# Kernel tuning notes

Measured on AMD Instinct MI355X. Metric: run time of the kernel, lower is better.

Reference implementation:

```python
import jax, jax.numpy as jnp
import numpy as np

EMBED_DIM = 1024
VOCAB = 32000
B, S = 4, 4096


def setup_inputs() -> dict:
    key = jax.random.key(0)
    ks = jax.random.split(key, 6)
    scale = 1.0 / np.sqrt(EMBED_DIM)
    x = jax.random.randint(ks[0], (B, S), 0, VOCAB, dtype=jnp.int64)
    embed = jax.random.normal(ks[1], (VOCAB, EMBED_DIM), dtype=jnp.float32)
    qkv_w = jax.random.normal(ks[2], (EMBED_DIM, 3 * EMBED_DIM), dtype=jnp.float32) * scale
    qkv_b = jnp.zeros((3 * EMBED_DIM,), dtype=jnp.float32)
    out_w = jax.random.normal(ks[3], (EMBED_DIM, VOCAB), dtype=jnp.float32) * scale
    out_b = jnp.zeros((VOCAB,), dtype=jnp.float32)
    return {"x": x, "embed": embed, "qkv_w": qkv_w, "qkv_b": qkv_b,
            "out_w": out_w, "out_b": out_b}


def reference(x, embed, qkv_w, qkv_b, out_w, out_b):
    h = embed[x]                                   # [B,S,D] token embedding lookup
    qkv = h @ qkv_w + qkv_b                        # [B,S,3D]
    qkv = qkv.reshape(B, S, 3, EMBED_DIM)
    q, k, v = qkv[:, :, 0], qkv[:, :, 1], qkv[:, :, 2]
    logits = jnp.einsum('bqd,bkd->bqk', q, k) / jnp.sqrt(jnp.float32(EMBED_DIM))
    attn = jax.nn.softmax(logits, axis=-1)         # [B,S,S] full score matrix (as in source)
    out = jnp.einsum('bqk,bkd->bqd', attn, v)
    h = out + h                                    # residual
    # source applies output projection then slices last token; equivalent to
    # projecting the last-token hidden only.
    return h[:, -1, :] @ out_w + out_b             # [B, vocab]
```

## Files before the change

kernel.cpp:

```cpp
#include <hip/hip_runtime.h>
#include <hip/hip_bf16.h>

typedef __bf16 bf16;
typedef __bf16 bf16x4 __attribute__((ext_vector_type(4)));
typedef __bf16 bf16x8 __attribute__((ext_vector_type(8)));
typedef float floatx4 __attribute__((ext_vector_type(4)));

#define EMBED 1024
#define VOCAB 32000
#define BB    4
#define SS    4096
#define NTOK  (BB * SS)
#define NKV   2048
#define NSEG  16

__device__ __forceinline__ void async_copy16(void* lds, const void* g) {
    __builtin_amdgcn_global_load_lds(
        (const __attribute__((address_space(1))) unsigned int*)g,
        (__attribute__((address_space(3))) unsigned int*)lds, 16, 0, 0);
}

__global__ void gather_embed(const int* __restrict__ x,
                             const float* __restrict__ embed,
                             bf16* __restrict__ h,
                             float* __restrict__ h_last,
                             float* __restrict__ h_final) {
    int t = blockIdx.x;
    int tid = threadIdx.x;
    int row = x[t];
    const float4* src = (const float4*)(embed + (size_t)row * EMBED);
    float4 v = src[tid];
    bf16x4 o; o.x = (bf16)v.x; o.y = (bf16)v.y; o.z = (bf16)v.z; o.w = (bf16)v.w;
    *(bf16x4*)(h + (size_t)t * EMBED + tid * 4) = o;
    if ((t & (SS - 1)) == SS - 1) {
        int b = t >> 12;
        *(float4*)(h_last  + b * EMBED + tid * 4) = v;
        *(float4*)(h_final + b * EMBED + tid * 4) = v;
    }
}

__global__ void wkvt_transpose(const float* __restrict__ qkv_w,
                               bf16* __restrict__ WkvT) {
    __shared__ float T[32][33];
    int n0 = blockIdx.x * 32, d0 = blockIdx.y * 32;
    int tid = threadIdx.x;
    int c = tid & 31, r = tid >> 5;
#pragma unroll
    for (int i = 0; i < 4; ++i) {
        int d = r + i * 8;
        T[c][d] = qkv_w[(size_t)(d0 + d) * (3 * EMBED) + EMBED + n0 + c];
    }
    __syncthreads();
#pragma unroll
    for (int i = 0; i < 4; ++i) {
        int n = r + i * 8;
        WkvT[(size_t)(n0 + n) * EMBED + d0 + c] = (bf16)T[n][c];
    }
}

__global__ void q_gemm(const float* __restrict__ h_last,
                       const float* __restrict__ qkv_w,
                       float* __restrict__ qpart) {
    __shared__ float hs[BB * 64];
    int tid = threadIdx.x;
    int seg = blockIdx.x, d0 = seg * 64;
    hs[tid] = h_last[(tid >> 6) * EMBED + d0 + (tid & 63)];
    __syncthreads();
    int j0 = tid * 4;
    floatx4 acc[BB];
#pragma unroll
    for (int b = 0; b < BB; ++b) acc[b] = (floatx4)0.0f;
#pragma unroll 4
    for (int dd = 0; dd < 64; ++dd) {
        float4 w = *(const float4*)(qkv_w + (size_t)(d0 + dd) * (3 * EMBED) + j0);
#pragma unroll
        for (int b = 0; b < BB; ++b) {
            float hv = hs[b * 64 + dd];
            acc[b][0] += hv * w.x; acc[b][1] += hv * w.y;
            acc[b][2] += hv * w.z; acc[b][3] += hv * w.w;
        }
    }
#pragma unroll
    for (int b = 0; b < BB; ++b)
        *(floatx4*)(qpart + ((size_t)seg * BB + b) * EMBED + j0) = acc[b];
}

__global__ void q_reduce(const float* __restrict__ qpart,
                         const float* __restrict__ qkv_b,
                         float* __restrict__ q) {
    int k = blockIdx.x * 256 + threadIdx.x;
    int b = k >> 10, d = k & (EMBED - 1);
    float s = qkv_b[d];
#pragma unroll
    for (int sg = 0; sg < NSEG; ++sg) s += qpart[((size_t)sg * BB + b) * EMBED + d];
    q[k] = s;
}

__global__ __launch_bounds__(512, 2) void gemm_kv(
    const bf16* __restrict__ A,
    const bf16* __restrict__ BT,
    const float* __restrict__ bias,
    bf16* __restrict__ C) {
    __shared__ __align__(16) bf16 SA[2][2][256 * 32];
    __shared__ __align__(16) bf16 SB[2][2][256 * 32];

    const int tid  = threadIdx.x;
    const int wave = tid >> 6, lane = tid & 63;
    const int wm = wave >> 2, wn = wave & 3;
    const int l16 = lane & 15, quad = lane >> 4;
    const int swz_l = (l16 & 3) ^ ((l16 >> 2) & 3);
    const int a_base = (wm * 128 + l16) * 32 + (quad ^ swz_l) * 8;
    const int b_base = (wn * 64  + l16) * 32 + (quad ^ swz_l) * 8;

    const bf16* Abase = A  + (size_t)blockIdx.x * 256 * EMBED;
    const bf16* Bbase = BT + (size_t)blockIdx.y * 256 * EMBED;

    floatx4 acc[8][4];
#pragma unroll
    for (int m = 0; m < 8; ++m)
#pragma unroll
        for (int n = 0; n < 4; ++n) acc[m][n] = (floatx4)0.0f;

    bf16x8 af[4], bfr[4];

#define STAGE_A(HALF, KT) do { \
    int c_ = wave * 128 + lane; \
    int r_ = c_ >> 2, sw_ = (r_ & 3) ^ ((r_ >> 2) & 3); \
    async_copy16(&SA[HALF][(KT) & 1][c_ * 8], \
        Abase + (size_t)r_ * EMBED + (KT) * 64 + (HALF) * 32 + ((c_ & 3) ^ sw_) * 8); \
    c_ += 64; r_ = c_ >> 2; sw_ = (r_ & 3) ^ ((r_ >> 2) & 3); \
    async_copy16(&SA[HALF][(KT) & 1][c_ * 8], \
        Abase + (size_t)r_ * EMBED + (KT) * 64 + (HALF) * 32 + ((c_ & 3) ^ sw_) * 8); \
} while (0)

#define STAGE_B(HALF, KT) do { \
    int c_ = wave * 128 + lane; \
    int r_ = c_ >> 2, sw_ = (r_ & 3) ^ ((r_ >> 2) & 3); \
    async_copy16(&SB[HALF][(KT) & 1][c_ * 8], \
        Bbase + (size_t)r_ * EMBED + (KT) * 64 + (HALF) * 32 + ((c_ & 3) ^ sw_) * 8); \
    c_ += 64; r_ = c_ >> 2; sw_ = (r_ & 3) ^ ((r_ >> 2) & 3); \
    async_copy16(&SB[HALF][(KT) & 1][c_ * 8], \
        Bbase + (size_t)r_ * EMBED + (KT) * 64 + (HALF) * 32 + ((c_ & 3) ^ sw_) * 8); \
} while (0)

#define RD_A(KS, PAR, MH) do { \
    const bf16* pa_ = &SA[KS][PAR][a_base + (MH) * 2048]; \
    _Pragma("unroll") \
    for (int mf_ = 0; mf_ < 4; ++mf_) af[mf_] = *(const bf16x8*)(pa_ + mf_ * 512); \
} while (0)

#define RD_B(KS, PAR) do { \
    const bf16* pb_ = &SB[KS][PAR][b_base]; \
    _Pragma("unroll") \
    for (int nf_ = 0; nf_ < 4; ++nf_) bfr[nf_] = *(const bf16x8*)(pb_ + nf_ * 512); \
} while (0)

#define MFMA16(MH) do { \
    __builtin_amdgcn_s_setprio(1); \
    _Pragma("unroll") \
    for (int mf_ = 0; mf_ < 4; ++mf_) \
    _Pragma("unroll") \
    for (int nf_ = 0; nf_ < 4; ++nf_) \
        acc[(MH) * 4 + mf_][nf_] = __builtin_amdgcn_mfma_f32_16x16x32_bf16( \
            af[mf_], bfr[nf_], acc[(MH) * 4 + mf_][nf_], 0, 0, 0); \
    __builtin_amdgcn_s_setprio(0); \
} while (0)

#define BARLG() do { __builtin_amdgcn_s_barrier(); \
    asm volatile("s_waitcnt lgkmcnt(0)" ::: "memory"); } while (0)
#define BAR()   __builtin_amdgcn_s_barrier()
#define WAIT8() do { __builtin_amdgcn_sched_barrier(0); \
    asm volatile("s_waitcnt vmcnt(8)" ::: "memory"); } while (0)
#define WAIT4() do { __builtin_amdgcn_sched_barrier(0); \
    asm volatile("s_waitcnt vmcnt(4)" ::: "memory"); } while (0)
#define WAIT0() do { __builtin_amdgcn_sched_barrier(0); \
    asm volatile("s_waitcnt vmcnt(0)" ::: "memory"); } while (0)
#define NOSTG() do { } while (0)

#define GROUP(PAR, S1, S2, S3, S4, W2, W4) do { \
    RD_A(0, PAR, 0); RD_B(0, PAR); S1; BARLG(); MFMA16(0); BAR(); \
    RD_A(0, PAR, 1);               S2; BARLG(); MFMA16(1); W2; BAR(); \
    RD_A(1, PAR, 0); RD_B(1, PAR); S3; BARLG(); MFMA16(0); BAR(); \
    RD_A(1, PAR, 1);               S4; BARLG(); MFMA16(1); W4; BAR(); \
} while (0)

    STAGE_A(0, 0); STAGE_B(0, 0);
    STAGE_A(1, 0); STAGE_B(1, 0);
    STAGE_A(0, 1); STAGE_B(0, 1);
    __builtin_amdgcn_sched_barrier(0);
    asm volatile("s_waitcnt vmcnt(8)" ::: "memory");
    BAR();

#pragma unroll 1
    for (int kk = 0; kk < 7; ++kk) {
        const int k0 = kk * 2, k1 = k0 + 1;
        GROUP(0, STAGE_A(1, k0 + 1), STAGE_B(1, k0 + 1),
                 STAGE_A(0, k0 + 2), STAGE_B(0, k0 + 2), WAIT8(), WAIT8());
        GROUP(1, STAGE_A(1, k1 + 1), STAGE_B(1, k1 + 1),
                 STAGE_A(0, k1 + 2), STAGE_B(0, k1 + 2), WAIT8(), WAIT8());
    }
    GROUP(0, STAGE_A(1, 15), STAGE_B(1, 15), NOSTG(), NOSTG(), WAIT8(), WAIT4());
    GROUP(1, NOSTG(), NOSTG(), NOSTG(), NOSTG(), WAIT0(), NOSTG());

    const int crow0 = blockIdx.x * 256 + wm * 128;
    const int ccol0 = blockIdx.y * 256 + wn * 64;
    float bsv[4];
#pragma unroll
    for (int nf = 0; nf < 4; ++nf) bsv[nf] = bias[ccol0 + nf * 16 + l16];
#pragma unroll
    for (int fm = 0; fm < 8; ++fm)
#pragma unroll
        for (int nf = 0; nf < 4; ++nf) {
            int col = ccol0 + nf * 16 + l16;
#pragma unroll
            for (int r = 0; r < 4; ++r) {
                int row = crow0 + fm * 16 + quad * 4 + r;
                C[(size_t)row * NKV + col] = (bf16)(acc[fm][nf][r] + bsv[nf]);
            }
        }
#undef STAGE_A
#undef STAGE_B
#undef RD_A
#undef RD_B
#undef MFMA16
#undef BARLG
#undef BAR
#undef WAIT8
#undef WAIT4
#undef WAIT0
#undef NOSTG
#undef GROUP
}

__global__ void attn_logits(const bf16* __restrict__ KV,
                            const float* __restrict__ q,
                            float* __restrict__ logits) {
    __shared__ float qs[EMBED];
    int b = blockIdx.x >> 10;
    int t = (blockIdx.x & 1023) * 4 + (threadIdx.x >> 6);
    int lane = threadIdx.x & 63;
    *(float4*)(qs + threadIdx.x * 4) = *(const float4*)(q + b * EMBED + threadIdx.x * 4);
    __syncthreads();
    const bf16* Krow = KV + (size_t)(b * SS + t) * NKV;
    float sum = 0.0f;
#pragma unroll
    for (int i = 0; i < 2; ++i) {
        int d0 = i * 512 + lane * 8;
        bf16x8 kv8 = *(const bf16x8*)(Krow + d0);
        float4 qa = *(const float4*)(qs + d0);
        float4 qc = *(const float4*)(qs + d0 + 4);
        sum += qa.x * (float)kv8[0] + qa.y * (float)kv8[1] +
               qa.z * (float)kv8[2] + qa.w * (float)kv8[3] +
               qc.x * (float)kv8[4] + qc.y * (float)kv8[5] +
               qc.z * (float)kv8[6] + qc.w * (float)kv8[7];
    }
#pragma unroll
    for (int o = 32; o; o >>= 1) sum += __shfl_down(sum, o);
    if (lane == 0) logits[b * SS + t] = sum * 0.03125f;
}

__global__ void softmax_k(const float* __restrict__ logits,
                          float* __restrict__ wts) {
    int b = blockIdx.x, tid = threadIdx.x;
    __shared__ float redm[16], reds[16];
    const float* l = logits + b * SS;
    float x0 = l[tid], x1 = l[tid + 1024], x2 = l[tid + 2048], x3 = l[tid + 3072];
    float m = fmaxf(fmaxf(x0, x1), fmaxf(x2, x3));
#pragma unroll
    for (int o = 32; o; o >>= 1) m = fmaxf(m, __shfl_down(m, o));
    if ((tid & 63) == 0) redm[tid >> 6] = m;
    __syncthreads();
    float M = redm[0];
#pragma unroll
    for (int i = 1; i < 16; ++i) M = fmaxf(M, redm[i]);
    float e0 = expf(x0 - M), e1 = expf(x1 - M), e2 = expf(x2 - M), e3 = expf(x3 - M);
    float s = e0 + e1 + e2 + e3;
#pragma unroll
    for (int o = 32; o; o >>= 1) s += __shfl_down(s, o);
    if ((tid & 63) == 0) reds[tid >> 6] = s;
    __syncthreads();
    float S = 0.0f;
#pragma unroll
    for (int i = 0; i < 16; ++i) S += reds[i];
    float inv = 1.0f / S;
    float* w = wts + b * SS;
    w[tid] = e0 * inv; w[tid + 1024] = e1 * inv;
    w[tid + 2048] = e2 * inv; w[tid + 3072] = e3 * inv;
}

__global__ void attn_av(const bf16* __restrict__ KV,
                        const float* __restrict__ wts,
                        float* __restrict__ avpart) {
    int b = blockIdx.x >> 6, ts = blockIdx.x & 63;
    int tid = threadIdx.x;
    __shared__ float wsh[64];
    if (tid < 64) wsh[tid] = wts[b * SS + ts * 64 + tid];
    __syncthreads();
    int d = tid * 4;
    const bf16* Vb = KV + (size_t)(b * SS + ts * 64) * NKV + EMBED + d;
    float a0 = 0, a1 = 0, a2 = 0, a3 = 0;
#pragma unroll 4
    for (int j = 0; j < 64; ++j) {
        bf16x4 v = *(const bf16x4*)(Vb + (size_t)j * NKV);
        float w = wsh[j];
        a0 += w * (float)v.x; a1 += w * (float)v.y;
        a2 += w * (float)v.z; a3 += w * (float)v.w;
    }
    float4 o; o.x = a0; o.y = a1; o.z = a2; o.w = a3;
    *(float4*)(avpart + (size_t)(b * 64 + ts) * EMBED + d) = o;
}

__global__ void av_reduce(const float* __restrict__ avpart,
                          float* __restrict__ h_final) {
    int i = blockIdx.x * 256 + threadIdx.x;
    int b = i >> 10, d = i & (EMBED - 1);
    float s = 0.0f;
#pragma unroll
    for (int ts = 0; ts < 64; ++ts)
        s += avpart[(size_t)(b * 64 + ts) * EMBED + d];
    h_final[i] += s;
}

__global__ void out_gemm(const float* __restrict__ h_final,
                         const float* __restrict__ out_w,
                         float* __restrict__ opart) {
    __shared__ float hs[BB * 64];
    int tid = threadIdx.x;
    int seg = blockIdx.y, d0 = seg * 64;
    hs[tid] = h_final[(tid >> 6) * EMBED + d0 + (tid & 63)];
    __syncthreads();
    int j0 = blockIdx.x * 1024 + tid * 4;
    if (j0 >= VOCAB) return;
    floatx4 acc[BB];
#pragma unroll
    for (int b = 0; b < BB; ++b) acc[b] = (floatx4)0.0f;
#pragma unroll 4
    for (int dd = 0; dd < 64; ++dd) {
        float4 w = *(const float4*)(out_w + (size_t)(d0 + dd) * VOCAB + j0);
#pragma unroll
        for (int b = 0; b < BB; ++b) {
            float hv = hs[b * 64 + dd];
            acc[b][0] += hv * w.x; acc[b][1] += hv * w.y;
            acc[b][2] += hv * w.z; acc[b][3] += hv * w.w;
        }
    }
#pragma unroll
    for (int b = 0; b < BB; ++b)
        *(floatx4*)(opart + ((size_t)seg * BB + b) * VOCAB + j0) = acc[b];
}

__global__ void out_reduce(const float* __restrict__ opart,
                           const float* __restrict__ out_b,
                           float* __restrict__ out) {
    int i = blockIdx.x * 256 + threadIdx.x;
    if (i >= BB * VOCAB) return;
    int b = i / VOCAB, j = i - b * VOCAB;
    float s = out_b[j];
#pragma unroll
    for (int sg = 0; sg < NSEG; ++sg) s += opart[((size_t)sg * BB + b) * VOCAB + j];
    out[i] = s;
}

extern "C" void kernel_launch(void* const* d_in, const int* in_sizes, int n_in,
                              void* d_out, int out_size, void* d_ws, size_t ws_size,
                              hipStream_t stream) {
    const int*   x      = (const int*)d_in[0];
    const float* embed  = (const float*)d_in[1];
    const float* qkv_w  = (const float*)d_in[2];
    const float* qkv_b  = (const float*)d_in[3];
    const float* out_w  = (const float*)d_in[4];
    const float* out_b  = (const float*)d_in[5];
    float* out = (float*)d_out;

    char* ws = (char*)d_ws;
    bf16*  h       = (bf16*)(ws);
    float* avpart  = (float*)(ws);
    float* opart   = (float*)(ws);
    bf16*  KV      = (bf16*)(ws + 33554432);
    bf16*  WkvT    = (bf16*)(ws + 100663296);
    float* h_last  = (float*)(ws + 104857600);
    float* h_final = (float*)(ws + 104873984);
    float* q       = (float*)(ws + 104890368);
    float* logits  = (float*)(ws + 104906752);
    float* wts     = (float*)(ws + 104972288);
    float* qpart   = (float*)(ws + 105037824);

    gather_embed<<<NTOK, 256, 0, stream>>>(x, embed, h, h_last, h_final);
    wkvt_transpose<<<dim3(64, 32), 256, 0, stream>>>(qkv_w, WkvT);
    q_gemm<<<NSEG, 256, 0, stream>>>(h_last, qkv_w, qpart);
    q_reduce<<<16, 256, 0, stream>>>(qpart, qkv_b, q);
    gemm_kv<<<dim3(NTOK / 256, NKV / 256), 512, 0, stream>>>(
        h, WkvT, qkv_b + EMBED, KV);
    attn_logits<<<SS, 256, 0, stream>>>(KV, q, logits);
    softmax_k<<<BB, 1024, 0, stream>>>(logits, wts);
    attn_av<<<256, 256, 0, stream>>>(KV, wts, avpart);
    av_reduce<<<16, 256, 0, stream>>>(avpart, h_final);
    out_gemm<<<dim3(32, NSEG), 256, 0, stream>>>(h_final, out_w, opart);
    out_reduce<<<(BB * VOCAB + 255) / 256, 256, 0, stream>>>(opart, out_b, out);
}
```

Baseline: 400.2 us.

## Restructure gemm_kv main loop into one barrier per k-half with 32 MFMAs

Restructures the K/V GEMM pipeline. Each k-half step now does one vmcnt wait and one barrier, then issues the next stage's loads, reads both A halves and B from LDS, and runs 32 MFMAs. The old scheme used two barriers per 16 MFMAs. Launch bounds drop to one block per CU, which frees registers for the extra A fragment but lowers occupancy. The aim is less barrier and sync overhead and longer uninterrupted MFMA runs.

New measurement: 404.2 us. About the same (+1.0%).

```diff
diff --git a/kernel.cpp b/kernel.cpp
--- a/kernel.cpp
+++ b/kernel.cpp
@@ -96,7 +96,7 @@
     q[k] = s;
 }
 
-__global__ __launch_bounds__(512, 2) void gemm_kv(
+__global__ __launch_bounds__(512, 1) void gemm_kv(
     const bf16* __restrict__ A,
     const bf16* __restrict__ BT,
     const float* __restrict__ bias,
@@ -121,86 +121,66 @@
 #pragma unroll
         for (int n = 0; n < 4; ++n) acc[m][n] = (floatx4)0.0f;
 
-    bf16x8 af[4], bfr[4];
-
-#define STAGE_A(HALF, KT) do { \
+    bf16x8 af[4], af2[4], bfr[4];
+
+#define STG(KH, KT) do { \
     int c_ = wave * 128 + lane; \
     int r_ = c_ >> 2, sw_ = (r_ & 3) ^ ((r_ >> 2) & 3); \
-    async_copy16(&SA[HALF][(KT) & 1][c_ * 8], \
-        Abase + (size_t)r_ * EMBED + (KT) * 64 + (HALF) * 32 + ((c_ & 3) ^ sw_) * 8); \
+    size_t go_ = (size_t)r_ * EMBED + (KT) * 64 + (KH) * 32 + ((c_ & 3) ^ sw_) * 8; \
+    async_copy16(&SA[KH][(KT) & 1][c_ * 8], Abase + go_); \
+    async_copy16(&SB[KH][(KT) & 1][c_ * 8], Bbase + go_); \
     c_ += 64; r_ = c_ >> 2; sw_ = (r_ & 3) ^ ((r_ >> 2) & 3); \
-    async_copy16(&SA[HALF][(KT) & 1][c_ * 8], \
-        Abase + (size_t)r_ * EMBED + (KT) * 64 + (HALF) * 32 + ((c_ & 3) ^ sw_) * 8); \
+    go_ = (size_t)r_ * EMBED + (KT) * 64 + (KH) * 32 + ((c_ & 3) ^ sw_) * 8; \
+    async_copy16(&SA[KH][(KT) & 1][c_ * 8], Abase + go_); \
+    async_copy16(&SB[KH][(KT) & 1][c_ * 8], Bbase + go_); \
 } while (0)
 
-#define STAGE_B(HALF, KT) do { \
-    int c_ = wave * 128 + lane; \
-    int r_ = c_ >> 2, sw_ = (r_ & 3) ^ ((r_ >> 2) & 3); \
-    async_copy16(&SB[HALF][(KT) & 1][c_ * 8], \
-        Bbase + (size_t)r_ * EMBED + (KT) * 64 + (HALF) * 32 + ((c_ & 3) ^ sw_) * 8); \
-    c_ += 64; r_ = c_ >> 2; sw_ = (r_ & 3) ^ ((r_ >> 2) & 3); \
-    async_copy16(&SB[HALF][(KT) & 1][c_ * 8], \
-        Bbase + (size_t)r_ * EMBED + (KT) * 64 + (HALF) * 32 + ((c_ & 3) ^ sw_) * 8); \
-} while (0)
-
-#define RD_A(KS, PAR, MH) do { \
-    const bf16* pa_ = &SA[KS][PAR][a_base + (MH) * 2048]; \
-    _Pragma("unroll") \
-    for (int mf_ = 0; mf_ < 4; ++mf_) af[mf_] = *(const bf16x8*)(pa_ + mf_ * 512); \
-} while (0)
-
-#define RD_B(KS, PAR) do { \
-    const bf16* pb_ = &SB[KS][PAR][b_base]; \
-    _Pragma("unroll") \
-    for (int nf_ = 0; nf_ < 4; ++nf_) bfr[nf_] = *(const bf16x8*)(pb_ + nf_ * 512); \
-} while (0)
-
-#define MFMA16(MH) do { \
+#define NOSTG() do { } while (0)
+
+#define HSTEP(KH, PAR, STG_BODY, WN) do { \
+    __builtin_amdgcn_sched_barrier(0); \
+    asm volatile("s_waitcnt vmcnt(" #WN ")" ::: "memory"); \
+    __builtin_amdgcn_s_barrier(); \
+    __builtin_amdgcn_sched_barrier(0); \
+    STG_BODY; \
+    { const bf16* pa_ = &SA[KH][PAR][a_base]; \
+      const bf16* pb_ = &SB[KH][PAR][b_base]; \
+      _Pragma("unroll") \
+      for (int i_ = 0; i_ < 4; ++i_) af [i_] = *(const bf16x8*)(pa_ + i_ * 512); \
+      _Pragma("unroll") \
+      for (int i_ = 0; i_ < 4; ++i_) bfr[i_] = *(const bf16x8*)(pb_ + i_ * 512); \
+      _Pragma("unroll") \
+      for (int i_ = 0; i_ < 4; ++i_) af2[i_] = *(const bf16x8*)(pa_ + 2048 + i_ * 512); } \
     __builtin_amdgcn_s_setprio(1); \
     _Pragma("unroll") \
     for (int mf_ = 0; mf_ < 4; ++mf_) \
     _Pragma("unroll") \
     for (int nf_ = 0; nf_ < 4; ++nf_) \
-        acc[(MH) * 4 + mf_][nf_] = __builtin_amdgcn_mfma_f32_16x16x32_bf16( \
-            af[mf_], bfr[nf_], acc[(MH) * 4 + mf_][nf_], 0, 0, 0); \
+        acc[mf_][nf_] = __builtin_amdgcn_mfma_f32_16x16x32_bf16( \
+            af[mf_], bfr[nf_], acc[mf_][nf_], 0, 0, 0); \
+    _Pragma("unroll") \
+    for (int mf_ = 0; mf_ < 4; ++mf_) \
+    _Pragma("unroll") \
+    for (int nf_ = 0; nf_ < 4; ++nf_) \
+        acc[4 + mf_][nf_] = __builtin_amdgcn_mfma_f32_16x16x32_bf16( \
+            af2[mf_], bfr[nf_], acc[4 + mf_][nf_], 0, 0, 0); \
     __builtin_amdgcn_s_setprio(0); \
 } while (0)
 
-#define BARLG() do { __builtin_amdgcn_s_barrier(); \
-    asm volatile("s_waitcnt lgkmcnt(0)" ::: "memory"); } while (0)
-#define BAR()   __builtin_amdgcn_s_barrier()
-#define WAIT8() do { __builtin_amdgcn_sched_barrier(0); \
-    asm volatile("s_waitcnt vmcnt(8)" ::: "memory"); } while (0)
-#define WAIT4() do { __builtin_amdgcn_sched_barrier(0); \
-    asm volatile("s_waitcnt vmcnt(4)" ::: "memory"); } while (0)
-#define WAIT0() do { __builtin_amdgcn_sched_barrier(0); \
-    asm volatile("s_waitcnt vmcnt(0)" ::: "memory"); } while (0)
-#define NOSTG() do { } while (0)
-
-#define GROUP(PAR, S1, S2, S3, S4, W2, W4) do { \
-    RD_A(0, PAR, 0); RD_B(0, PAR); S1; BARLG(); MFMA16(0); BAR(); \
-    RD_A(0, PAR, 1);               S2; BARLG(); MFMA16(1); W2; BAR(); \
-    RD_A(1, PAR, 0); RD_B(1, PAR); S3; BARLG(); MFMA16(0); BAR(); \
-    RD_A(1, PAR, 1);               S4; BARLG(); MFMA16(1); W4; BAR(); \
-} while (0)
-
-    STAGE_A(0, 0); STAGE_B(0, 0);
-    STAGE_A(1, 0); STAGE_B(1, 0);
-    STAGE_A(0, 1); STAGE_B(0, 1);
-    __builtin_amdgcn_sched_barrier(0);
-    asm volatile("s_waitcnt vmcnt(8)" ::: "memory");
-    BAR();
+    STG(0, 0); STG(1, 0); STG(0, 1);
 
 #pragma unroll 1
     for (int kk = 0; kk < 7; ++kk) {
-        const int k0 = kk * 2, k1 = k0 + 1;
-        GROUP(0, STAGE_A(1, k0 + 1), STAGE_B(1, k0 + 1),
-                 STAGE_A(0, k0 + 2), STAGE_B(0, k0 + 2), WAIT8(), WAIT8());
-        GROUP(1, STAGE_A(1, k1 + 1), STAGE_B(1, k1 + 1),
-                 STAGE_A(0, k1 + 2), STAGE_B(0, k1 + 2), WAIT8(), WAIT8());
-    }
-    GROUP(0, STAGE_A(1, 15), STAGE_B(1, 15), NOSTG(), NOSTG(), WAIT8(), WAIT4());
-    GROUP(1, NOSTG(), NOSTG(), NOSTG(), NOSTG(), WAIT0(), NOSTG());
+        const int t1 = 2 * kk + 1;
+        HSTEP(0, 0, STG(1, t1),     8);
+        HSTEP(1, 0, STG(0, t1 + 1), 8);
+        HSTEP(0, 1, STG(1, t1 + 1), 8);
+        HSTEP(1, 1, STG(0, t1 + 2), 8);
+    }
+    HSTEP(0, 0, STG(1, 15), 8);
+    HSTEP(1, 0, NOSTG(),    8);
+    HSTEP(0, 1, NOSTG(),    4);
+    HSTEP(1, 1, NOSTG(),    0);
 
     const int crow0 = blockIdx.x * 256 + wm * 128;
     const int ccol0 = blockIdx.y * 256 + wn * 64;
@@ -218,18 +198,9 @@
                 C[(size_t)row * NKV + col] = (bf16)(acc[fm][nf][r] + bsv[nf]);
             }
         }
-#undef STAGE_A
-#undef STAGE_B
-#undef RD_A
-#undef RD_B
-#undef MFMA16
-#undef BARLG
-#undef BAR
-#undef WAIT8
-#undef WAIT4
-#undef WAIT0
+#undef STG
 #undef NOSTG
-#undef GROUP
+#undef HSTEP
 }
 
 __global__ void attn_logits(const bf16* __restrict__ KV,
```
